# Optimization experiments

Hardware: AMD Instinct MI355X
Metric: run time of the kernel (lower is better)

## Reference

```python
import jax, jax.numpy as jnp
import numpy as np

# irreps: input = 32x0e + 16x1o (dim 80); key/query/value = 8x0e + 4x1o (dim 20); lmax = 1
N_NODES = 10000
N_EDGES = 160000
MUL0_IN, MUL1_IN = 32, 16
MUL0_OUT, MUL1_OUT = 8, 4
NUM_BASIS = 32
HIDDEN = 32
MAX_RADIUS = 2.5
NUM_NEIGHBORS = 32
# per-edge fully-connected TP weight blocks (paths: 0e*0e->0e, 1o*1o->0e, 0e*1o->1o, 1o*0e->1o)
S00 = MUL0_IN * MUL0_OUT    # 256
S110 = MUL1_IN * MUL0_OUT   # 128
S01 = MUL0_IN * MUL1_OUT    # 128
S10 = MUL1_IN * MUL1_OUT    # 64
WNUMEL = S00 + S110 + S01 + S10  # 576
SQRT3 = 1.7320508075688772


def _split_irreps(z, mul0, mul1):
    return z[:, :mul0], z[:, mul0:].reshape(-1, mul1, 3)


def _basis_net(rb, w1, w2):
    # e3nn FullyConnectedNet([num_basis, 32, weight_numel], silu): x @ W / sqrt(fan_in)
    h = jax.nn.silu(rb @ w1 / jnp.sqrt(float(NUM_BASIS)))
    return h @ w2 / jnp.sqrt(float(HIDDEN))


def _edge_tp(x0, x1, Y1, w):
    # FullyConnectedTensorProduct with per-edge weights w [E, WNUMEL].
    # e3nn component/element normalization: path_weight = sqrt(dim(ir_out)/fan_in),
    # fan_in per output irrep = MUL0_IN + MUL1_IN = 48; CG(1,1,0)=CG(0,1,1)=delta/sqrt(3).
    c = 1.0 / jnp.sqrt(float(MUL0_IN + MUL1_IN))
    w00 = w[:, :S00].reshape(-1, MUL0_IN, MUL0_OUT)
    w110 = w[:, S00:S00 + S110].reshape(-1, MUL1_IN, MUL0_OUT)
    w01 = w[:, S00 + S110:S00 + S110 + S01].reshape(-1, MUL0_IN, MUL1_OUT)
    w10 = w[:, S00 + S110 + S01:].reshape(-1, MUL1_IN, MUL1_OUT)
    x1dotY = jnp.einsum('eum,em->eu', x1, Y1)  # [E, MUL1_IN]
    out0 = c * (jnp.einsum('euw,eu->ew', w00, x0)
                + jnp.einsum('euw,eu->ew', w110, x1dotY) / SQRT3)
    out1 = c * (jnp.einsum('euw,eu->ew', w01, x0)[:, :, None] * Y1[:, None, :]
                + jnp.einsum('euw,eum->ewm', w10, x1))
    return out0, out1  # [E, MUL0_OUT], [E, MUL1_OUT, 3]


def _forward(x, pos, w_q0, w_q1, w_kb1, w_kb2, w_vb1, w_vb2, w_sim0, w_sim1, edge_index):
    src, dst = edge_index[0], edge_index[1]
    vec = pos[src] - pos[dst]                                   # [E,3]
    r = jnp.sqrt(jnp.sum(vec * vec, axis=1) + 1e-24)            # [E]
    # bessel soft_one_hot_linspace (cutoff=True), scaled by sqrt(num_basis)
    n = jnp.arange(1, NUM_BASIS + 1, dtype=jnp.float32)
    rb = jnp.sqrt(2.0 / MAX_RADIUS) * jnp.sin(n * jnp.pi * r[:, None] / MAX_RADIUS) / r[:, None]
    rb = rb * jnp.sqrt(float(NUM_BASIS))
    # soft_unit_step(10*(1 - r/max_radius)) = exp(-1/t) for t > 0 else 0
    t = 10.0 * (1.0 - r / MAX_RADIUS)
    cutoff = jnp.where(t > 0.0, jnp.exp(-1.0 / jnp.maximum(t, 1e-12)), 0.0)
    # spherical harmonics lmax=1, 'component' norm: Y0 = 1, Y1 = sqrt(3)*unit_vec
    Y1 = SQRT3 * vec / r[:, None]
    x0, x1 = _split_irreps(x, MUL0_IN, MUL1_IN)
    # o3.Linear query projection: independent per-l blocks, / sqrt(fan_in)
    q0 = x0 @ w_q0 / jnp.sqrt(float(MUL0_IN))                   # [N,8]
    q1 = jnp.einsum('num,uw->nwm', x1, w_q1) / jnp.sqrt(float(MUL1_IN))  # [N,4,3]
    wk = _basis_net(rb, w_kb1, w_kb2)                           # [E,576]
    wv = _basis_net(rb, w_vb1, w_vb2)                           # [E,576]
    x0s, x1s = x0[src], x1[src]
    k0, k1 = _edge_tp(x0s, x1s, Y1, wk)
    v0, v1 = _edge_tp(x0s, x1s, Y1, wv)
    # similarity TP (query x key -> 0e): fan_in = 8*8 + 4*4 = 80
    cs = 1.0 / jnp.sqrt(float(MUL0_OUT ** 2 + MUL1_OUT ** 2))
    sim = cs * (jnp.einsum('uv,eu,ev->e', w_sim0, q0[src], k0)
                + jnp.einsum('uv,eum,evm->e', w_sim1, q1[src], k1) / SQRT3)
    logits = cutoff * sim
    # segment softmax grouped by src node
    m = jax.ops.segment_max(logits, src, num_segments=N_NODES)
    m = jnp.where(jnp.isfinite(m), m, 0.0)
    ex = jnp.exp(logits - m[src])
    den = jax.ops.segment_sum(ex, src, num_segments=N_NODES)
    attn = ex / den[src]                                        # [E]
    a = jnp.sqrt(jax.nn.relu(attn))[:, None]                    # [E,1]
    vals = jnp.concatenate([v0, v1.reshape(-1, MUL1_OUT * 3)], axis=1)  # [E,20]
    return jax.ops.segment_sum(a * vals, dst, num_segments=N_NODES) / NUM_NEIGHBORS


def setup_inputs():
    key = jax.random.key(0)
    ks = jax.random.split(key, 11)
    return {
        'x': jax.random.normal(ks[0], (N_NODES, MUL0_IN + 3 * MUL1_IN), jnp.float32),
        'pos': jax.random.uniform(ks[1], (N_NODES, 3), jnp.float32) * MAX_RADIUS,
        'w_q0': jax.random.normal(ks[2], (MUL0_IN, MUL0_OUT), jnp.float32),
        'w_q1': jax.random.normal(ks[3], (MUL1_IN, MUL1_OUT), jnp.float32),
        'w_kb1': jax.random.normal(ks[4], (NUM_BASIS, HIDDEN), jnp.float32),
        'w_kb2': jax.random.normal(ks[5], (HIDDEN, WNUMEL), jnp.float32),
        'w_vb1': jax.random.normal(ks[6], (NUM_BASIS, HIDDEN), jnp.float32),
        'w_vb2': jax.random.normal(ks[7], (HIDDEN, WNUMEL), jnp.float32),
        'w_sim0': jax.random.normal(ks[8], (MUL0_OUT, MUL0_OUT), jnp.float32),
        'w_sim1': jax.random.normal(ks[9], (MUL1_OUT, MUL1_OUT), jnp.float32),
        'edge_index': jax.random.randint(ks[10], (2, N_EDGES), 0, N_NODES, dtype=jnp.int32),
    }


def reference(x, pos, w_q0, w_q1, w_kb1, w_kb2, w_vb1, w_vb2, w_sim0, w_sim1, edge_index):
    return _forward(x, pos, w_q0, w_q1, w_kb1, w_kb2, w_vb1, w_vb2, w_sim0, w_sim1, edge_index)
```

## Files before the change

kernel.cpp:

```cpp
#include <hip/hip_runtime.h>
#include <hip/hip_fp16.h>
#include <math.h>

#define NN 10000
#define NE 160000

typedef _Float16 half8 __attribute__((ext_vector_type(8)));
typedef __attribute__((ext_vector_type(4))) float f32x4;

constexpr float SQRT3f    = 1.7320508075688772f;
constexpr float ISQRT3    = 0.57735026918962576f;
constexpr float ISQRT32   = 0.17677669529663687f;
constexpr float C_TP      = 0.14433756729740645f;
constexpr float CSIM      = 0.11180339887498949f;
constexpr float PREB      = 5.0596442562694074f;
constexpr float PI_OVER_R = 1.2566370614359172f;
constexpr float INV_RMAX  = 0.4f;
constexpr float HKSC      = C_TP * ISQRT32;
constexpr float DEN_SCALE = 16777216.0f;
constexpr float DEN_INV   = 1.0f / 16777216.0f;
constexpr float OUT_SCALE = 8388608.0f;
constexpr float OUT_INV   = 1.0f / 8388608.0f;

__device__ __forceinline__ unsigned fkey(float f) {
  unsigned u = __float_as_uint(f);
  return (u & 0x80000000u) ? ~u : (u | 0x80000000u);
}
__device__ __forceinline__ float funkey(unsigned k) {
  return (k & 0x80000000u) ? __uint_as_float(k ^ 0x80000000u)
                           : __uint_as_float(~k);
}
__device__ __forceinline__ unsigned short f2h(float f) {
  return __half_as_ushort(__float2half(f));
}

__device__ __forceinline__ int origcol(int n) {
  if (n >= 576) return 512 + (n - 576);
  int w = n / 48, u = n % 48;
  if (w < 8) return (u < 32) ? (u * 8 + w) : (256 + (u - 32) * 8 + w);
  return (u < 32) ? (384 + u * 4 + (w - 8)) : -1;
}

__global__ void __launch_bounds__(256) k_prep(
    const float* __restrict__ w_vb1, const float* __restrict__ w_vb2,
    float* __restrict__ W1vt, unsigned short* __restrict__ Wtv)
{
  int tid = blockIdx.x * 256 + threadIdx.x;
  if (tid < 640 * 32) {
    int n = tid / 32, h = tid % 32;
    int oc = origcol(n);
    float v = (oc >= 0) ? w_vb2[h * 576 + oc] : 0.0f;
    Wtv[n * 32 + h] = f2h(v);
  }
  if (tid < 1024) {
    int h = tid / 32, n2 = tid % 32;
    W1vt[h * 32 + n2] = w_vb1[n2 * 32 + h];
  }
}

__global__ void __launch_bounds__(256) k_node(
    const float* __restrict__ x, const float* __restrict__ w_q0,
    const float* __restrict__ w_q1, const float* __restrict__ w_sim0,
    const float* __restrict__ w_sim1,
    float* __restrict__ qs0, float* __restrict__ qs1)
{
  int n = blockIdx.x * 256 + threadIdx.x;
  if (n >= NN) return;
  float x0[32], x1f[48];
  const float4* xr = (const float4*)(x + 80 * n);
#pragma unroll
  for (int i = 0; i < 8; ++i) {
    float4 v = xr[i];
    x0[4*i]=v.x; x0[4*i+1]=v.y; x0[4*i+2]=v.z; x0[4*i+3]=v.w;
  }
#pragma unroll
  for (int i = 0; i < 12; ++i) {
    float4 v = xr[8 + i];
    x1f[4*i]=v.x; x1f[4*i+1]=v.y; x1f[4*i+2]=v.z; x1f[4*i+3]=v.w;
  }
  float q0[8];
#pragma unroll
  for (int w = 0; w < 8; ++w) {
    float a = 0.f;
#pragma unroll
    for (int u = 0; u < 32; ++u) a = fmaf(x0[u], w_q0[u * 8 + w], a);
    q0[w] = a * ISQRT32;
  }
  float q1[12];
#pragma unroll
  for (int w = 0; w < 4; ++w)
#pragma unroll
    for (int m = 0; m < 3; ++m) {
      float a = 0.f;
#pragma unroll
      for (int u = 0; u < 16; ++u) a = fmaf(x1f[3*u+m], w_q1[u*4+w], a);
      q1[w * 3 + m] = a * 0.25f;
    }
#pragma unroll
  for (int v = 0; v < 8; ++v) {
    float a = 0.f;
#pragma unroll
    for (int u = 0; u < 8; ++u) a = fmaf(w_sim0[u * 8 + v], q0[u], a);
    qs0[n * 8 + v] = CSIM * a;
  }
#pragma unroll
  for (int v = 0; v < 4; ++v)
#pragma unroll
    for (int m = 0; m < 3; ++m) {
      float a = 0.f;
#pragma unroll
      for (int u = 0; u < 4; ++u) a = fmaf(w_sim1[u*4+v], q1[u*3+m], a);
      qs1[n * 12 + v * 3 + m] = (CSIM * ISQRT3) * a;
    }
}

__global__ void __launch_bounds__(256) k_edge(
    const float* __restrict__ pos,
    const int* __restrict__ esrc, const int* __restrict__ edst,
    const float* __restrict__ W1vt,
    unsigned* __restrict__ hvo, float* __restrict__ geom,
    float* __restrict__ rbuf)
{
  int e = blockIdx.x * 256 + threadIdx.x;
  if (e >= NE) return;
  int s = esrc[e], d = edst[e];
  float vx = pos[3*s]   - pos[3*d];
  float vy = pos[3*s+1] - pos[3*d+1];
  float vz = pos[3*s+2] - pos[3*d+2];
  float r = sqrtf(fmaf(vx, vx, fmaf(vy, vy, vz * vz)) + 1e-24f);
  float inv_r = 1.0f / r;

  float rb[32];
  {
    float sn, cth;
    sincosf(PI_OVER_R * r, &sn, &cth);
    float twoc = 2.0f * cth, pre = PREB * inv_r, snm1 = 0.0f;
#pragma unroll
    for (int n = 0; n < 32; ++n) {
      rb[n] = pre * sn;
      float t = fmaf(twoc, sn, -snm1);
      snm1 = sn; sn = t;
    }
  }
  float Yx = SQRT3f * vx * inv_r, Yy = SQRT3f * vy * inv_r, Yz = SQRT3f * vz * inv_r;
  float tc = 10.0f * (1.0f - r * INV_RMAX);
  float cut = (tc > 0.0f) ? __expf(-1.0f / tc) : 0.0f;
  *(float4*)(geom + 4 * e) = make_float4(Yx, Yy, Yz, cut);
  rbuf[e] = r;

#pragma unroll 1
  for (int h = 0; h < 32; h += 2) {
    const float* wv0 = W1vt + h * 32;
    const float* wv1 = W1vt + (h + 1) * 32;
    float av0 = 0.f, av1 = 0.f;
#pragma unroll
    for (int n = 0; n < 32; ++n) {
      float rn = rb[n];
      av0 = fmaf(rn, wv0[n], av0);
      av1 = fmaf(rn, wv1[n], av1);
    }
    av0 *= ISQRT32; av1 *= ISQRT32;
    float hv0 = av0 / (1.0f + __expf(-av0)) * HKSC;
    float hv1 = av1 / (1.0f + __expf(-av1)) * HKSC;
    hvo[e * 16 + (h >> 1)] = (unsigned)f2h(hv0) | ((unsigned)f2h(hv1) << 16);
  }
}

template <int HALF>
__global__ void __launch_bounds__(256) k_nodeF(
    const float* __restrict__ x, const float* __restrict__ w_kb2,
    const float* __restrict__ qs0g, const float* __restrict__ qs1g,
    float* __restrict__ nodeF)
{
  __shared__ float W2f[16 * 577];
  __shared__ float ndl[16][100];

  const int tid = threadIdx.x;
  const int nb = blockIdx.x * 16;

#pragma unroll
  for (int i = 0; i < 36; ++i) {
    int idx = i * 256 + tid;
    int row = idx / 576, col = idx - row * 576;
    W2f[row * 577 + col] = w_kb2[(HALF * 16 + row) * 576 + col];
  }
  for (int j = tid; j < 1600; j += 256) {
    int nn = j / 100, jj = j - nn * 100;
    int n = nb + nn;
    float v;
    if (jj < 80)      v = x[80 * n + jj];
    else if (jj < 88) v = qs0g[8 * n + (jj - 80)];
    else              v = qs1g[12 * n + (jj - 88)];
    ndl[nn][jj] = v;
  }
  __syncthreads();

  const int nn = tid >> 4, hh = tid & 15;
  const float* Wh = W2f + hh * 577;
  const float* nd = ndl[nn];

  float t14 = 0.f;
#pragma unroll
  for (int a = 0; a < 32; ++a) {
    float tmp = 0.f;
#pragma unroll
    for (int v = 0; v < 8; ++v) tmp = fmaf(Wh[a * 8 + v], nd[80 + v], tmp);
    t14 = fmaf(tmp, nd[a], t14);
  }
#pragma unroll
  for (int a = 0; a < 16; ++a)
#pragma unroll
    for (int v = 0; v < 4; ++v) {
      float dotv = fmaf(nd[32 + 3*a], nd[88 + 3*v],
                   fmaf(nd[32 + 3*a + 1], nd[88 + 3*v + 1],
                        nd[32 + 3*a + 2] * nd[88 + 3*v + 2]));
      t14 = fmaf(Wh[512 + a * 4 + v], dotv, t14);
    }

  float F0 = 0.f, F1 = 0.f, F2 = 0.f;
#pragma unroll
  for (int a = 0; a < 16; ++a) {
    float q = 0.f;
#pragma unroll
    for (int v = 0; v < 8; ++v) q = fmaf(Wh[256 + a * 8 + v], nd[80 + v], q);
    F0 = fmaf(q, nd[32 + 3*a],     F0);
    F1 = fmaf(q, nd[32 + 3*a + 1], F1);
    F2 = fmaf(q, nd[32 + 3*a + 2], F2);
  }
  F0 *= ISQRT3; F1 *= ISQRT3; F2 *= ISQRT3;
#pragma unroll
  for (int v = 0; v < 4; ++v) {
    float rr = 0.f;
#pragma unroll
    for (int a = 0; a < 32; ++a) rr = fmaf(Wh[384 + a * 4 + v], nd[a], rr);
    F0 = fmaf(rr, nd[88 + 3*v],     F0);
    F1 = fmaf(rr, nd[88 + 3*v + 1], F1);
    F2 = fmaf(rr, nd[88 + 3*v + 2], F2);
  }

  const int n = nb + nn, h = HALF * 16 + hh;
  *(float4*)(nodeF + (size_t)(n * 32 + h) * 4) = make_float4(t14, F0, F1, F2);
}

__global__ void __launch_bounds__(256) k_elogit(
    const float* __restrict__ rbuf, const float* __restrict__ geom,
    const int* __restrict__ esrc, const float* __restrict__ w_kb1,
    const float* __restrict__ nodeF,
    float* __restrict__ logits, unsigned* __restrict__ mkey)
{
  __shared__ float W1s[32 * 33];
  const int tid = threadIdx.x;
#pragma unroll
  for (int i = 0; i < 4; ++i) {
    int idx = i * 256 + tid;
    W1s[(idx >> 5) * 33 + (idx & 31)] = w_kb1[idx];
  }
  __syncthreads();

  const int e = blockIdx.x * 256 + tid;
  if (e >= NE) return;
  const int s = esrc[e];
  const float r = rbuf[e];
  const float4 g4 = *(const float4*)(geom + 4 * e);

  float rb[32];
  {
    float sn, cth;
    sincosf(PI_OVER_R * r, &sn, &cth);
    float twoc = 2.0f * cth, pre = PREB / r, snm1 = 0.0f;
#pragma unroll
    for (int n = 0; n < 32; ++n) {
      rb[n] = pre * sn;
      float t = fmaf(twoc, sn, -snm1);
      snm1 = sn; sn = t;
    }
  }

  const float4* nf = (const float4*)(nodeF + (size_t)s * 128);
  float sim = 0.f;
#pragma unroll 1
  for (int h = 0; h < 32; ++h) {
    float ak = 0.f;
#pragma unroll
    for (int n = 0; n < 32; ++n) ak = fmaf(rb[n], W1s[n * 33 + h], ak);
    ak *= ISQRT32;
    float hk = ak / (1.0f + __expf(-ak)) * HKSC;
    float4 f = nf[h];
    float S = fmaf(f.y, g4.x, fmaf(f.z, g4.y, fmaf(f.w, g4.z, f.x)));
    sim = fmaf(hk, S, sim);
  }
  float lg = g4.w * sim;
  logits[e] = lg;
  atomicMax(mkey + s, fkey(lg));
}

__global__ void __launch_bounds__(256) k_den(
    const float* __restrict__ logits, const int* __restrict__ esrc,
    const unsigned* __restrict__ mkey,
    float* __restrict__ exb, int* __restrict__ deni)
{
  int e = blockIdx.x * 256 + threadIdx.x;
  if (e >= NE) return;
  int s = esrc[e];
  float m = funkey(mkey[s]);
  float ex = expf(logits[e] - m);
  exb[e] = ex;
  atomicAdd(&deni[s], __float2int_rn(ex * DEN_SCALE));
}

__global__ void __launch_bounds__(256) k_tpv(
    const unsigned short* __restrict__ hmat, const unsigned short* __restrict__ Wt,
    const float* __restrict__ x, const float* __restrict__ geom,
    const int* __restrict__ esrc, const int* __restrict__ edst,
    const float* __restrict__ exb, const int* __restrict__ deni,
    int* __restrict__ outi)
{
  __shared__ __align__(16) uint4  wlds4[2304];
  __shared__ __align__(16) float g_lds[4][16 * 52];
  __shared__ __align__(16) float x1_lds[4][16 * 52];

  const int l = threadIdx.x & 63, wv = threadIdx.x >> 6;
  const int tile = blockIdx.x * 4 + wv;
  const int G = l >> 4, c = l & 15;
  const int ebase = tile * 16;

  const uint4* Wt4 = (const uint4*)Wt;
#pragma unroll
  for (int i = 0; i < 9; ++i) {
    int chunk = i * 256 + threadIdx.x;
    wlds4[chunk] = Wt4[chunk];
  }

#pragma unroll
  for (int i = 0; i < 5; ++i) {
    int idx = i * 64 + l;
    int ee = idx / 20, q = idx - 20 * ee;
    int ss = esrc[ebase + ee];
    float4 v = *(const float4*)(x + 80 * ss + 4 * q);
    if (q < 8)
      *(float4*)(&g_lds[wv][ee * 52 + 4 * q]) = v;
    else
      *(float4*)(&x1_lds[wv][ee * 52 + 4 * q - 32]) = v;
  }
  {
    int ee = l >> 2, ug = l & 3;
    int ss = esrc[ebase + ee];
    float4 gm = *(const float4*)(geom + 4 * (ebase + ee));
    const float* xp = x + 80 * ss + 32 + 12 * ug;
    float4 p0 = *(const float4*)(xp);
    float4 p1 = *(const float4*)(xp + 4);
    float4 p2 = *(const float4*)(xp + 8);
    float4 o;
    o.x = ISQRT3 * fmaf(p0.x, gm.x, fmaf(p0.y, gm.y, p0.z * gm.z));
    o.y = ISQRT3 * fmaf(p0.w, gm.x, fmaf(p1.x, gm.y, p1.y * gm.z));
    o.z = ISQRT3 * fmaf(p1.z, gm.x, fmaf(p1.w, gm.y, p2.x * gm.z));
    o.w = ISQRT3 * fmaf(p2.y, gm.x, fmaf(p2.z, gm.y, p2.w * gm.z));
    *(float4*)(&g_lds[wv][ee * 52 + 32 + 4 * ug]) = o;
  }

  half8 a8 = *(const half8*)(hmat + (ebase + c) * 32 + 8 * G);

  __syncthreads();

  half8 bt[4];
#pragma unroll
  for (int t = 0; t < 4; ++t)
    bt[t] = *(const half8*)(Wt + ((36 + t) * 16 + c) * 32 + 8 * G);

  float vacc[4][12];
#pragma unroll
  for (int r = 0; r < 4; ++r)
#pragma unroll
    for (int w = 0; w < 12; ++w) vacc[r][w] = 0.0f;
  float ot1[4][3];
#pragma unroll
  for (int r = 0; r < 4; ++r) { ot1[r][0]=0.f; ot1[r][1]=0.f; ot1[r][2]=0.f; }

  const f32x4 zero4 = {0.f, 0.f, 0.f, 0.f};
#pragma unroll
  for (int t = 0; t < 36; ++t) {
    union { uint4 u; half8 h; } cvt;
    cvt.u = wlds4[(t * 16 + c) * 4 + G];
    f32x4 dd = __builtin_amdgcn_mfma_f32_16x16x32_f16(a8, cvt.h, zero4, 0, 0, 0);
    const int w = t / 3, u0 = (t % 3) * 16;
#pragma unroll
    for (int r = 0; r < 4; ++r)
      vacc[r][w] = fmaf(dd[r], g_lds[wv][(4 * G + r) * 52 + u0 + c], vacc[r][w]);
  }
#pragma unroll
  for (int t = 0; t < 4; ++t) {
    f32x4 dd = __builtin_amdgcn_mfma_f32_16x16x32_f16(a8, bt[t], zero4, 0, 0, 0);
    const int u = 4 * t + (c >> 2);
#pragma unroll
    for (int r = 0; r < 4; ++r) {
      const float* xp = &x1_lds[wv][(4 * G + r) * 52 + 3 * u];
      ot1[r][0] = fmaf(dd[r], xp[0], ot1[r][0]);
      ot1[r][1] = fmaf(dd[r], xp[1], ot1[r][1]);
      ot1[r][2] = fmaf(dd[r], xp[2], ot1[r][2]);
    }
  }

#pragma unroll
  for (int m = 1; m < 16; m <<= 1)
#pragma unroll
    for (int r = 0; r < 4; ++r)
#pragma unroll
      for (int w = 0; w < 12; ++w)
        vacc[r][w] += __shfl_xor(vacc[r][w], m);
#pragma unroll
  for (int m = 4; m < 16; m <<= 1)
#pragma unroll
    for (int r = 0; r < 4; ++r)
#pragma unroll
      for (int k = 0; k < 3; ++k)
        ot1[r][k] += __shfl_xor(ot1[r][k], m);

  float treg[4] = {0.f, 0.f, 0.f, 0.f};
#pragma unroll
  for (int w = 0; w < 12; ++w)
    if (c == w) {
#pragma unroll
      for (int r = 0; r < 4; ++r) treg[r] = vacc[r][w];
    }

  int sr[4]; float4 g4[4];
#pragma unroll
  for (int r = 0; r < 4; ++r) {
    sr[r] = esrc[ebase + 4 * G + r];
    g4[r] = *(const float4*)(geom + 4 * (ebase + 4 * G + r));
  }

  float a_[4]; int dst[4];
#pragma unroll
  for (int r = 0; r < 4; ++r) {
    int eg = ebase + 4 * G + r;
    dst[r] = edst[eg];
    float denf = (float)deni[sr[r]] * DEN_INV;
    a_[r] = sqrtf(fmaxf(exb[eg] / denf, 0.f)) * 0.03125f;
  }
  float s01w[4];
#pragma unroll
  for (int r = 0; r < 4; ++r) s01w[r] = __shfl_xor(treg[r], 8);
  if (c < 8) {
#pragma unroll
    for (int r = 0; r < 4; ++r)
      atomicAdd(outi + 20 * dst[r] + c,
                __float2int_rn(a_[r] * treg[r] * OUT_SCALE));
  }
  if (c < 4) {
#pragma unroll
    for (int r = 0; r < 4; ++r) {
      float vx_ = fmaf(s01w[r], g4[r].x, ot1[r][0]);
      float vy_ = fmaf(s01w[r], g4[r].y, ot1[r][1]);
      float vz_ = fmaf(s01w[r], g4[r].z, ot1[r][2]);
      atomicAdd(outi + 20 * dst[r] + 8 + 3 * c + 0,
                __float2int_rn(a_[r] * vx_ * OUT_SCALE));
      atomicAdd(outi + 20 * dst[r] + 8 + 3 * c + 1,
                __float2int_rn(a_[r] * vy_ * OUT_SCALE));
      atomicAdd(outi + 20 * dst[r] + 8 + 3 * c + 2,
                __float2int_rn(a_[r] * vz_ * OUT_SCALE));
    }
  }
}

__global__ void __launch_bounds__(256) k_out(
    const int* __restrict__ outi, float* __restrict__ out)
{
  int i = blockIdx.x * 256 + threadIdx.x;
  if (i < NN * 20) out[i] = (float)outi[i] * OUT_INV;
}

extern "C" void kernel_launch(void* const* d_in, const int* in_sizes, int n_in,
                              void* d_out, int out_size, void* d_ws, size_t ws_size,
                              hipStream_t stream)
{
  const float* x      = (const float*)d_in[0];
  const float* pos    = (const float*)d_in[1];
  const float* w_q0   = (const float*)d_in[2];
  const float* w_q1   = (const float*)d_in[3];
  const float* w_kb1  = (const float*)d_in[4];
  const float* w_kb2  = (const float*)d_in[5];
  const float* w_vb1  = (const float*)d_in[6];
  const float* w_vb2  = (const float*)d_in[7];
  const float* w_sim0 = (const float*)d_in[8];
  const float* w_sim1 = (const float*)d_in[9];
  const int*   eidx   = (const int*)d_in[10];
  const int* esrc = eidx;
  const int* edst = eidx + NE;
  float* out = (float*)d_out;

  float* ws      = (float*)d_ws;
  float* geom    = ws;
  float* rbuf    = geom + (size_t)NE * 4;
  float* qs0     = rbuf + NE;
  float* qs1     = qs0 + NN * 8;
  float* logits  = qs1 + NN * 12;
  float* exb     = logits + NE;
  float* W1vt    = exb + NE;
  float* nodeF   = W1vt + 1024;
  int*   deni    = (int*)(nodeF + (size_t)NN * 128);
  unsigned* mkey = (unsigned*)(deni + NN);
  int*   outi    = (int*)(mkey + NN);
  unsigned short* hv  = (unsigned short*)(outi + NN * 20);
  unsigned short* Wtv = hv + (size_t)NE * 32;

  hipMemsetAsync(deni, 0, (size_t)(NN * 22) * sizeof(int), stream);

  const int eb = (NE + 255) / 256;
  k_prep<<<dim3((640 * 32 + 255) / 256), dim3(256), 0, stream>>>(
      w_vb1, w_vb2, W1vt, Wtv);
  k_node<<<dim3((NN + 255) / 256), dim3(256), 0, stream>>>(
      x, w_q0, w_q1, w_sim0, w_sim1, qs0, qs1);
  k_edge<<<dim3(eb), dim3(256), 0, stream>>>(
      pos, esrc, edst, W1vt, (unsigned*)hv, geom, rbuf);
  k_nodeF<0><<<dim3(NN / 16), dim3(256), 0, stream>>>(
      x, w_kb2, qs0, qs1, nodeF);
  k_nodeF<1><<<dim3(NN / 16), dim3(256), 0, stream>>>(
      x, w_kb2, qs0, qs1, nodeF);
  k_elogit<<<dim3(eb), dim3(256), 0, stream>>>(
      rbuf, geom, esrc, w_kb1, nodeF, logits, mkey);
  k_den<<<dim3(eb), dim3(256), 0, stream>>>(logits, esrc, mkey, exb, deni);
  k_tpv<<<dim3(NE / 64), dim3(256), 0, stream>>>(
      hv, Wtv, x, geom, esrc, edst, exb, deni, outi);
  k_out<<<dim3((NN * 20 + 255) / 256), dim3(256), 0, stream>>>(outi, out);
}
```

Baseline: 184.5 us.

## Fuse edge geometry and logit kernels, transpose hidden layout, use fp16 LDS in TPV

Merges the edge-geometry/value-hidden kernel with the key-logit kernel, so the radial Bessel basis is computed once and the rbuf round trip and one launch disappear. The key first-layer weights are pre-transposed in the prep kernel and read from global memory (likely cached) instead of LDS. The value hidden activations are stored in a transposed [16][NE] packed-half layout. The TPV kernel now keeps node features in fp16 LDS and hoists the per-row gate values into registers. These changes add register pressure in the fused kernel and some precision loss from fp16 staging of x.

```diff
diff --git a/kernel.cpp b/kernel.cpp
--- a/kernel.cpp
+++ b/kernel.cpp
@@ -43,18 +43,24 @@
 
 __global__ void __launch_bounds__(256) k_prep(
     const float* __restrict__ w_vb1, const float* __restrict__ w_vb2,
-    float* __restrict__ W1vt, unsigned short* __restrict__ Wtv)
+    const float* __restrict__ w_kb1,
+    float* __restrict__ W1vt, float* __restrict__ W1kt,
+    unsigned short* __restrict__ Wtv)
 {
   int tid = blockIdx.x * 256 + threadIdx.x;
   if (tid < 640 * 32) {
-    int n = tid / 32, h = tid % 32;
+    int n = tid >> 5, h = tid & 31;
     int oc = origcol(n);
     float v = (oc >= 0) ? w_vb2[h * 576 + oc] : 0.0f;
     Wtv[n * 32 + h] = f2h(v);
   }
   if (tid < 1024) {
-    int h = tid / 32, n2 = tid % 32;
+    int h = tid >> 5, n2 = tid & 31;
     W1vt[h * 32 + n2] = w_vb1[n2 * 32 + h];
+  } else if (tid < 2048) {
+    int j = tid - 1024;
+    int h = j >> 5, n2 = j & 31;
+    W1kt[h * 32 + n2] = w_kb1[n2 * 32 + h];
   }
 }
 
@@ -114,12 +120,89 @@
     }
 }
 
-__global__ void __launch_bounds__(256) k_edge(
+template <int HALF>
+__global__ void __launch_bounds__(256) k_nodeF(
+    const float* __restrict__ x, const float* __restrict__ w_kb2,
+    const float* __restrict__ qs0g, const float* __restrict__ qs1g,
+    float* __restrict__ nodeF)
+{
+  __shared__ float W2f[16 * 577];
+  __shared__ float ndl[16][100];
+
+  const int tid = threadIdx.x;
+  const int nb = blockIdx.x * 16;
+
+#pragma unroll
+  for (int i = 0; i < 36; ++i) {
+    int idx = i * 256 + tid;
+    int row = idx / 576, col = idx - row * 576;
+    W2f[row * 577 + col] = w_kb2[(HALF * 16 + row) * 576 + col];
+  }
+  for (int j = tid; j < 1600; j += 256) {
+    int nn = j / 100, jj = j - nn * 100;
+    int n = nb + nn;
+    float v;
+    if (jj < 80)      v = x[80 * n + jj];
+    else if (jj < 88) v = qs0g[8 * n + (jj - 80)];
+    else              v = qs1g[12 * n + (jj - 88)];
+    ndl[nn][jj] = v;
+  }
+  __syncthreads();
+
+  const int nn = tid >> 4, hh = tid & 15;
+  const float* Wh = W2f + hh * 577;
+  const float* nd = ndl[nn];
+
+  float t14 = 0.f;
+#pragma unroll
+  for (int a = 0; a < 32; ++a) {
+    float tmp = 0.f;
+#pragma unroll
+    for (int v = 0; v < 8; ++v) tmp = fmaf(Wh[a * 8 + v], nd[80 + v], tmp);
+    t14 = fmaf(tmp, nd[a], t14);
+  }
+#pragma unroll
+  for (int a = 0; a < 16; ++a)
+#pragma unroll
+    for (int v = 0; v < 4; ++v) {
+      float dotv = fmaf(nd[32 + 3*a], nd[88 + 3*v],
+                   fmaf(nd[32 + 3*a + 1], nd[88 + 3*v + 1],
+                        nd[32 + 3*a + 2] * nd[88 + 3*v + 2]));
+      t14 = fmaf(Wh[512 + a * 4 + v], dotv, t14);
+    }
+
+  float F0 = 0.f, F1 = 0.f, F2 = 0.f;
+#pragma unroll
+  for (int a = 0; a < 16; ++a) {
+    float q = 0.f;
+#pragma unroll
+    for (int v = 0; v < 8; ++v) q = fmaf(Wh[256 + a * 8 + v], nd[80 + v], q);
+    F0 = fmaf(q, nd[32 + 3*a],     F0);
+    F1 = fmaf(q, nd[32 + 3*a + 1], F1);
+    F2 = fmaf(q, nd[32 + 3*a + 2], F2);
+  }
+  F0 *= ISQRT3; F1 *= ISQRT3; F2 *= ISQRT3;
+#pragma unroll
+  for (int v = 0; v < 4; ++v) {
+    float rr = 0.f;
+#pragma unroll
+    for (int a = 0; a < 32; ++a) rr = fmaf(Wh[384 + a * 4 + v], nd[a], rr);
+    F0 = fmaf(rr, nd[88 + 3*v],     F0);
+    F1 = fmaf(rr, nd[88 + 3*v + 1], F1);
+    F2 = fmaf(rr, nd[88 + 3*v + 2], F2);
+  }
+
+  const int n = nb + nn, h = HALF * 16 + hh;
+  *(float4*)(nodeF + (size_t)(n * 32 + h) * 4) = make_float4(t14, F0, F1, F2);
+}
+
+__global__ void __launch_bounds__(256) k_edgelogit(
     const float* __restrict__ pos,
     const int* __restrict__ esrc, const int* __restrict__ edst,
-    const float* __restrict__ W1vt,
-    unsigned* __restrict__ hvo, float* __restrict__ geom,
-    float* __restrict__ rbuf)
+    const float* __restrict__ W1vt, const float* __restrict__ W1kt,
+    const float* __restrict__ nodeF,
+    unsigned* __restrict__ hv2, float* __restrict__ geom,
+    float* __restrict__ logits, unsigned* __restrict__ mkey)
 {
   int e = blockIdx.x * 256 + threadIdx.x;
   if (e >= NE) return;
@@ -146,150 +229,36 @@
   float tc = 10.0f * (1.0f - r * INV_RMAX);
   float cut = (tc > 0.0f) ? __expf(-1.0f / tc) : 0.0f;
   *(float4*)(geom + 4 * e) = make_float4(Yx, Yy, Yz, cut);
-  rbuf[e] = r;
-
+
+  const float4* nf = (const float4*)(nodeF) + (size_t)s * 32;
+  float sim = 0.f;
 #pragma unroll 1
-  for (int h = 0; h < 32; h += 2) {
-    const float* wv0 = W1vt + h * 32;
-    const float* wv1 = W1vt + (h + 1) * 32;
-    float av0 = 0.f, av1 = 0.f;
+  for (int h2 = 0; h2 < 16; ++h2) {
+    const float* wv0 = W1vt + (2 * h2) * 32;
+    const float* wv1 = wv0 + 32;
+    const float* wk0 = W1kt + (2 * h2) * 32;
+    const float* wk1 = wk0 + 32;
+    float av0 = 0.f, av1 = 0.f, ak0 = 0.f, ak1 = 0.f;
 #pragma unroll
     for (int n = 0; n < 32; ++n) {
       float rn = rb[n];
       av0 = fmaf(rn, wv0[n], av0);
       av1 = fmaf(rn, wv1[n], av1);
-    }
-    av0 *= ISQRT32; av1 *= ISQRT32;
+      ak0 = fmaf(rn, wk0[n], ak0);
+      ak1 = fmaf(rn, wk1[n], ak1);
+    }
+    av0 *= ISQRT32; av1 *= ISQRT32; ak0 *= ISQRT32; ak1 *= ISQRT32;
     float hv0 = av0 / (1.0f + __expf(-av0)) * HKSC;
     float hv1 = av1 / (1.0f + __expf(-av1)) * HKSC;
-    hvo[e * 16 + (h >> 1)] = (unsigned)f2h(hv0) | ((unsigned)f2h(hv1) << 16);
-  }
-}
-
-template <int HALF>
-__global__ void __launch_bounds__(256) k_nodeF(
-    const float* __restrict__ x, const float* __restrict__ w_kb2,
-    const float* __restrict__ qs0g, const float* __restrict__ qs1g,
-    float* __restrict__ nodeF)
-{
-  __shared__ float W2f[16 * 577];
-  __shared__ float ndl[16][100];
-
-  const int tid = threadIdx.x;
-  const int nb = blockIdx.x * 16;
-
-#pragma unroll
-  for (int i = 0; i < 36; ++i) {
-    int idx = i * 256 + tid;
-    int row = idx / 576, col = idx - row * 576;
-    W2f[row * 577 + col] = w_kb2[(HALF * 16 + row) * 576 + col];
-  }
-  for (int j = tid; j < 1600; j += 256) {
-    int nn = j / 100, jj = j - nn * 100;
-    int n = nb + nn;
-    float v;
-    if (jj < 80)      v = x[80 * n + jj];
-    else if (jj < 88) v = qs0g[8 * n + (jj - 80)];
-    else              v = qs1g[12 * n + (jj - 88)];
-    ndl[nn][jj] = v;
-  }
-  __syncthreads();
-
-  const int nn = tid >> 4, hh = tid & 15;
-  const float* Wh = W2f + hh * 577;
-  const float* nd = ndl[nn];
-
-  float t14 = 0.f;
-#pragma unroll
-  for (int a = 0; a < 32; ++a) {
-    float tmp = 0.f;
-#pragma unroll
-    for (int v = 0; v < 8; ++v) tmp = fmaf(Wh[a * 8 + v], nd[80 + v], tmp);
-    t14 = fmaf(tmp, nd[a], t14);
-  }
-#pragma unroll
-  for (int a = 0; a < 16; ++a)
-#pragma unroll
-    for (int v = 0; v < 4; ++v) {
-      float dotv = fmaf(nd[32 + 3*a], nd[88 + 3*v],
-                   fmaf(nd[32 + 3*a + 1], nd[88 + 3*v + 1],
-                        nd[32 + 3*a + 2] * nd[88 + 3*v + 2]));
-      t14 = fmaf(Wh[512 + a * 4 + v], dotv, t14);
-    }
-
-  float F0 = 0.f, F1 = 0.f, F2 = 0.f;
-#pragma unroll
-  for (int a = 0; a < 16; ++a) {
-    float q = 0.f;
-#pragma unroll
-    for (int v = 0; v < 8; ++v) q = fmaf(Wh[256 + a * 8 + v], nd[80 + v], q);
-    F0 = fmaf(q, nd[32 + 3*a],     F0);
-    F1 = fmaf(q, nd[32 + 3*a + 1], F1);
-    F2 = fmaf(q, nd[32 + 3*a + 2], F2);
-  }
-  F0 *= ISQRT3; F1 *= ISQRT3; F2 *= ISQRT3;
-#pragma unroll
-  for (int v = 0; v < 4; ++v) {
-    float rr = 0.f;
-#pragma unroll
-    for (int a = 0; a < 32; ++a) rr = fmaf(Wh[384 + a * 4 + v], nd[a], rr);
-    F0 = fmaf(rr, nd[88 + 3*v],     F0);
-    F1 = fmaf(rr, nd[88 + 3*v + 1], F1);
-    F2 = fmaf(rr, nd[88 + 3*v + 2], F2);
-  }
-
-  const int n = nb + nn, h = HALF * 16 + hh;
-  *(float4*)(nodeF + (size_t)(n * 32 + h) * 4) = make_float4(t14, F0, F1, F2);
-}
-
-__global__ void __launch_bounds__(256) k_elogit(
-    const float* __restrict__ rbuf, const float* __restrict__ geom,
-    const int* __restrict__ esrc, const float* __restrict__ w_kb1,
-    const float* __restrict__ nodeF,
-    float* __restrict__ logits, unsigned* __restrict__ mkey)
-{
-  __shared__ float W1s[32 * 33];
-  const int tid = threadIdx.x;
-#pragma unroll
-  for (int i = 0; i < 4; ++i) {
-    int idx = i * 256 + tid;
-    W1s[(idx >> 5) * 33 + (idx & 31)] = w_kb1[idx];
-  }
-  __syncthreads();
-
-  const int e = blockIdx.x * 256 + tid;
-  if (e >= NE) return;
-  const int s = esrc[e];
-  const float r = rbuf[e];
-  const float4 g4 = *(const float4*)(geom + 4 * e);
-
-  float rb[32];
-  {
-    float sn, cth;
-    sincosf(PI_OVER_R * r, &sn, &cth);
-    float twoc = 2.0f * cth, pre = PREB / r, snm1 = 0.0f;
-#pragma unroll
-    for (int n = 0; n < 32; ++n) {
-      rb[n] = pre * sn;
-      float t = fmaf(twoc, sn, -snm1);
-      snm1 = sn; sn = t;
-    }
-  }
-
-  const float4* nf = (const float4*)(nodeF + (size_t)s * 128);
-  float sim = 0.f;
-#pragma unroll 1
-  for (int h = 0; h < 32; ++h) {
-    float ak = 0.f;
-#pragma unroll
-    for (int n = 0; n < 32; ++n) ak = fmaf(rb[n], W1s[n * 33 + h], ak);
-    ak *= ISQRT32;
-    float hk = ak / (1.0f + __expf(-ak)) * HKSC;
-    float4 f = nf[h];
-    float S = fmaf(f.y, g4.x, fmaf(f.z, g4.y, fmaf(f.w, g4.z, f.x)));
-    sim = fmaf(hk, S, sim);
-  }
-  float lg = g4.w * sim;
+    hv2[(size_t)h2 * NE + e] = (unsigned)f2h(hv0) | ((unsigned)f2h(hv1) << 16);
+    float hk0 = ak0 / (1.0f + __expf(-ak0)) * HKSC;
+    float hk1 = ak1 / (1.0f + __expf(-ak1)) * HKSC;
+    float4 f0 = nf[2 * h2], f1 = nf[2 * h2 + 1];
+    float S0 = fmaf(f0.y, Yx, fmaf(f0.z, Yy, fmaf(f0.w, Yz, f0.x)));
+    float S1 = fmaf(f1.y, Yx, fmaf(f1.z, Yy, fmaf(f1.w, Yz, f1.x)));
+    sim = fmaf(hk0, S0, fmaf(hk1, S1, sim));
+  }
+  float lg = cut * sim;
   logits[e] = lg;
   atomicMax(mkey + s, fkey(lg));
 }
@@ -309,38 +278,40 @@
 }
 
 __global__ void __launch_bounds__(256) k_tpv(
-    const unsigned short* __restrict__ hmat, const unsigned short* __restrict__ Wt,
+    const unsigned* __restrict__ hv2, const unsigned short* __restrict__ Wtv,
     const float* __restrict__ x, const float* __restrict__ geom,
     const int* __restrict__ esrc, const int* __restrict__ edst,
     const float* __restrict__ exb, const int* __restrict__ deni,
     int* __restrict__ outi)
 {
-  __shared__ __align__(16) uint4  wlds4[2304];
-  __shared__ __align__(16) float g_lds[4][16 * 52];
-  __shared__ __align__(16) float x1_lds[4][16 * 52];
+  __shared__ __align__(16) unsigned short Bls[18432];
+  __shared__ __align__(16) _Float16 g_lds[4][16 * 52];
+  __shared__ __align__(16) _Float16 x1_lds[4][16 * 52];
 
   const int l = threadIdx.x & 63, wv = threadIdx.x >> 6;
-  const int tile = blockIdx.x * 4 + wv;
   const int G = l >> 4, c = l & 15;
-  const int ebase = tile * 16;
-
-  const uint4* Wt4 = (const uint4*)Wt;
-#pragma unroll
-  for (int i = 0; i < 9; ++i) {
-    int chunk = i * 256 + threadIdx.x;
-    wlds4[chunk] = Wt4[chunk];
-  }
-
+  const int ebase = (blockIdx.x * 4 + wv) * 16;
+
+  {
+    const uint4* src = (const uint4*)Wtv;
+    uint4* dst4 = (uint4*)Bls;
+#pragma unroll
+    for (int i = 0; i < 9; ++i)
+      dst4[i * 256 + threadIdx.x] = src[i * 256 + threadIdx.x];
+  }
+  union H4 { _Float16 h[4]; unsigned long long u; };
 #pragma unroll
   for (int i = 0; i < 5; ++i) {
     int idx = i * 64 + l;
     int ee = idx / 20, q = idx - 20 * ee;
     int ss = esrc[ebase + ee];
     float4 v = *(const float4*)(x + 80 * ss + 4 * q);
+    H4 p; p.h[0] = (_Float16)v.x; p.h[1] = (_Float16)v.y;
+    p.h[2] = (_Float16)v.z; p.h[3] = (_Float16)v.w;
     if (q < 8)
-      *(float4*)(&g_lds[wv][ee * 52 + 4 * q]) = v;
+      *(unsigned long long*)(&g_lds[wv][ee * 52 + 4 * q]) = p.u;
     else
-      *(float4*)(&x1_lds[wv][ee * 52 + 4 * q - 32]) = v;
+      *(unsigned long long*)(&x1_lds[wv][ee * 52 + 4 * q - 32]) = p.u;
   }
   {
     int ee = l >> 2, ug = l & 3;
@@ -350,22 +321,32 @@
     float4 p0 = *(const float4*)(xp);
     float4 p1 = *(const float4*)(xp + 4);
     float4 p2 = *(const float4*)(xp + 8);
-    float4 o;
-    o.x = ISQRT3 * fmaf(p0.x, gm.x, fmaf(p0.y, gm.y, p0.z * gm.z));
-    o.y = ISQRT3 * fmaf(p0.w, gm.x, fmaf(p1.x, gm.y, p1.y * gm.z));
-    o.z = ISQRT3 * fmaf(p1.z, gm.x, fmaf(p1.w, gm.y, p2.x * gm.z));
-    o.w = ISQRT3 * fmaf(p2.y, gm.x, fmaf(p2.z, gm.y, p2.w * gm.z));
-    *(float4*)(&g_lds[wv][ee * 52 + 32 + 4 * ug]) = o;
-  }
-
-  half8 a8 = *(const half8*)(hmat + (ebase + c) * 32 + 8 * G);
+    H4 o;
+    o.h[0] = (_Float16)(ISQRT3 * fmaf(p0.x, gm.x, fmaf(p0.y, gm.y, p0.z * gm.z)));
+    o.h[1] = (_Float16)(ISQRT3 * fmaf(p0.w, gm.x, fmaf(p1.x, gm.y, p1.y * gm.z)));
+    o.h[2] = (_Float16)(ISQRT3 * fmaf(p1.z, gm.x, fmaf(p1.w, gm.y, p2.x * gm.z)));
+    o.h[3] = (_Float16)(ISQRT3 * fmaf(p2.y, gm.x, fmaf(p2.z, gm.y, p2.w * gm.z)));
+    *(unsigned long long*)(&g_lds[wv][ee * 52 + 32 + 4 * ug]) = o.u;
+  }
+  union { unsigned u[4]; half8 h8; } ua;
+#pragma unroll
+  for (int j = 0; j < 4; ++j)
+    ua.u[j] = hv2[(size_t)(4 * G + j) * NE + ebase + c];
+  half8 a8 = ua.h8;
 
   __syncthreads();
 
   half8 bt[4];
 #pragma unroll
   for (int t = 0; t < 4; ++t)
-    bt[t] = *(const half8*)(Wt + ((36 + t) * 16 + c) * 32 + 8 * G);
+    bt[t] = *(const half8*)(Wtv + ((36 + t) * 16 + c) * 32 + 8 * G);
+
+  float gh[4][3];
+#pragma unroll
+  for (int r = 0; r < 4; ++r)
+#pragma unroll
+    for (int j = 0; j < 3; ++j)
+      gh[r][j] = (float)g_lds[wv][(4 * G + r) * 52 + 16 * j + c];
 
   float vacc[4][12];
 #pragma unroll
@@ -380,12 +361,12 @@
 #pragma unroll
   for (int t = 0; t < 36; ++t) {
     union { uint4 u; half8 h; } cvt;
-    cvt.u = wlds4[(t * 16 + c) * 4 + G];
+    cvt.u = *(const uint4*)(Bls + (t * 16 + c) * 32 + 8 * G);
     f32x4 dd = __builtin_amdgcn_mfma_f32_16x16x32_f16(a8, cvt.h, zero4, 0, 0, 0);
-    const int w = t / 3, u0 = (t % 3) * 16;
+    const int w = t / 3, j = t % 3;
 #pragma unroll
     for (int r = 0; r < 4; ++r)
-      vacc[r][w] = fmaf(dd[r], g_lds[wv][(4 * G + r) * 52 + u0 + c], vacc[r][w]);
+      vacc[r][w] = fmaf(dd[r], gh[r][j], vacc[r][w]);
   }
 #pragma unroll
   for (int t = 0; t < 4; ++t) {
@@ -393,10 +374,10 @@
     const int u = 4 * t + (c >> 2);
 #pragma unroll
     for (int r = 0; r < 4; ++r) {
-      const float* xp = &x1_lds[wv][(4 * G + r) * 52 + 3 * u];
-      ot1[r][0] = fmaf(dd[r], xp[0], ot1[r][0]);
-      ot1[r][1] = fmaf(dd[r], xp[1], ot1[r][1]);
-      ot1[r][2] = fmaf(dd[r], xp[2], ot1[r][2]);
+      const _Float16* xp = &x1_lds[wv][(4 * G + r) * 52 + 3 * u];
+      ot1[r][0] = fmaf(dd[r], (float)xp[0], ot1[r][0]);
+      ot1[r][1] = fmaf(dd[r], (float)xp[1], ot1[r][1]);
+      ot1[r][2] = fmaf(dd[r], (float)xp[2], ot1[r][2]);
     }
   }
 
@@ -423,18 +404,13 @@
       for (int r = 0; r < 4; ++r) treg[r] = vacc[r][w];
     }
 
-  int sr[4]; float4 g4[4];
-#pragma unroll
-  for (int r = 0; r < 4; ++r) {
-    sr[r] = esrc[ebase + 4 * G + r];
-    g4[r] = *(const float4*)(geom + 4 * (ebase + 4 * G + r));
-  }
-
-  float a_[4]; int dst[4];
+  int sr[4], dst[4]; float4 g4[4]; float a_[4];
 #pragma unroll
   for (int r = 0; r < 4; ++r) {
     int eg = ebase + 4 * G + r;
+    sr[r] = esrc[eg];
     dst[r] = edst[eg];
+    g4[r] = *(const float4*)(geom + 4 * eg);
     float denf = (float)deni[sr[r]] * DEN_INV;
     a_[r] = sqrtf(fmaxf(exb[eg] / denf, 0.f)) * 0.03125f;
   }
@@ -491,36 +467,34 @@
 
   float* ws      = (float*)d_ws;
   float* geom    = ws;
-  float* rbuf    = geom + (size_t)NE * 4;
-  float* qs0     = rbuf + NE;
+  float* qs0     = geom + (size_t)NE * 4;
   float* qs1     = qs0 + NN * 8;
   float* logits  = qs1 + NN * 12;
   float* exb     = logits + NE;
-  float* W1vt    = exb + NE;
-  float* nodeF   = W1vt + 1024;
-  int*   deni    = (int*)(nodeF + (size_t)NN * 128);
+  float* nodeF   = exb + NE;
+  float* W1vt    = nodeF + (size_t)NN * 128;
+  float* W1kt    = W1vt + 1024;
+  int*   deni    = (int*)(W1kt + 1024);
   unsigned* mkey = (unsigned*)(deni + NN);
   int*   outi    = (int*)(mkey + NN);
-  unsigned short* hv  = (unsigned short*)(outi + NN * 20);
-  unsigned short* Wtv = hv + (size_t)NE * 32;
+  unsigned* hv2  = (unsigned*)(outi + NN * 20);
+  unsigned short* Wtv = (unsigned short*)(hv2 + (size_t)16 * NE);
 
   hipMemsetAsync(deni, 0, (size_t)(NN * 22) * sizeof(int), stream);
 
   const int eb = (NE + 255) / 256;
-  k_prep<<<dim3((640 * 32 + 255) / 256), dim3(256), 0, stream>>>(
-      w_vb1, w_vb2, W1vt, Wtv);
+  k_prep<<<dim3(80), dim3(256), 0, stream>>>(
+      w_vb1, w_vb2, w_kb1, W1vt, W1kt, Wtv);
   k_node<<<dim3((NN + 255) / 256), dim3(256), 0, stream>>>(
       x, w_q0, w_q1, w_sim0, w_sim1, qs0, qs1);
-  k_edge<<<dim3(eb), dim3(256), 0, stream>>>(
-      pos, esrc, edst, W1vt, (unsigned*)hv, geom, rbuf);
   k_nodeF<0><<<dim3(NN / 16), dim3(256), 0, stream>>>(
       x, w_kb2, qs0, qs1, nodeF);
   k_nodeF<1><<<dim3(NN / 16), dim3(256), 0, stream>>>(
       x, w_kb2, qs0, qs1, nodeF);
-  k_elogit<<<dim3(eb), dim3(256), 0, stream>>>(
-      rbuf, geom, esrc, w_kb1, nodeF, logits, mkey);
+  k_edgelogit<<<dim3(eb), dim3(256), 0, stream>>>(
+      pos, esrc, edst, W1vt, W1kt, nodeF, hv2, geom, logits, mkey);
   k_den<<<dim3(eb), dim3(256), 0, stream>>>(logits, esrc, mkey, exb, deni);
   k_tpv<<<dim3(NE / 64), dim3(256), 0, stream>>>(
-      hv, Wtv, x, geom, esrc, edst, exb, deni, outi);
+      hv2, Wtv, x, geom, esrc, edst, exb, deni, outi);
   k_out<<<dim3((NN * 20 + 255) / 256), dim3(256), 0, stream>>>(outi, out);
 }
```

New measurement: 199.5 us. 8.1% more time.
